# Optimization experiments

Measured on AMD Instinct MI355X. Metric: run time of the kernel, lower is better.

## Reference

```python
import jax, jax.numpy as jnp
import numpy as np

H = 8          # num_heads
EPS = 1e-5     # nn.LayerNorm default eps


def _attn(x, kv, wq, bq, wk, bk, wv, bv, wo, bo):
    # x: [B, Nq, D] queries; kv: [B, Nk, D] keys/values. softmax over keys (dim=-1).
    B, Nq, D = x.shape
    Nk = kv.shape[1]
    d = D // H
    q = (x @ wq + bq).reshape(B, Nq, H, d).transpose(0, 2, 1, 3)   # [B,h,Nq,d]
    k = (kv @ wk + bk).reshape(B, Nk, H, d).transpose(0, 2, 1, 3)  # [B,h,Nk,d]
    v = (kv @ wv + bv).reshape(B, Nk, H, d).transpose(0, 2, 1, 3)  # [B,h,Nk,d]
    scores = jnp.einsum('bhqd,bhkd->bhqk', q, k) * (d ** -0.5)
    a = jax.nn.softmax(scores, axis=-1)                            # softmax_dim='keys'
    ctx = jnp.einsum('bhqk,bhkd->bhqd', a, v)
    ctx = ctx.transpose(0, 2, 1, 3).reshape(B, Nq, D)
    return ctx @ wo + bo


def _ln(x, g, b):
    mu = jnp.mean(x, axis=-1, keepdims=True)
    var = jnp.var(x, axis=-1, keepdims=True)  # biased, matches torch LayerNorm
    return (x - mu) * jax.lax.rsqrt(var + EPS) * g + b


def setup_inputs() -> dict:
    key = jax.random.key(0)
    B, Nq, Nk, D = 2, 2048, 4096, 512
    Hid = 4 * D
    ks = jax.random.split(key, 32)
    s = 0.02
    r = lambda i, shp: jax.random.normal(ks[i], shp, dtype=jnp.float32) * s
    inp = {
        'x': jax.random.normal(ks[0], (B, Nq, D), dtype=jnp.float32),
        'cross': jax.random.normal(ks[1], (B, Nk, D), dtype=jnp.float32),
        # cross-attention projections (stored as [in, out])
        'ca_wq': r(2, (D, D)), 'ca_bq': jnp.zeros((D,), jnp.float32),
        'ca_wk': r(3, (D, D)), 'ca_bk': jnp.zeros((D,), jnp.float32),
        'ca_wv': r(4, (D, D)), 'ca_bv': jnp.zeros((D,), jnp.float32),
        'ca_wo': r(5, (D, D)), 'ca_bo': jnp.zeros((D,), jnp.float32),
        # self-attention projections
        'sa_wq': r(6, (D, D)), 'sa_bq': jnp.zeros((D,), jnp.float32),
        'sa_wk': r(7, (D, D)), 'sa_bk': jnp.zeros((D,), jnp.float32),
        'sa_wv': r(8, (D, D)), 'sa_bv': jnp.zeros((D,), jnp.float32),
        'sa_wo': r(9, (D, D)), 'sa_bo': jnp.zeros((D,), jnp.float32),
        # layer norms
        'ln1_g': jnp.ones((D,), jnp.float32), 'ln1_b': jnp.zeros((D,), jnp.float32),
        'ln2_g': jnp.ones((D,), jnp.float32), 'ln2_b': jnp.zeros((D,), jnp.float32),
        # MLP
        'mlp_w1': r(10, (D, Hid)), 'mlp_b1': jnp.zeros((Hid,), jnp.float32),
        'mlp_w2': r(11, (Hid, D)), 'mlp_b2': jnp.zeros((D,), jnp.float32),
    }
    return inp


def reference(x, cross,
              ca_wq, ca_bq, ca_wk, ca_bk, ca_wv, ca_bv, ca_wo, ca_bo,
              sa_wq, sa_bq, sa_wk, sa_bk, sa_wv, sa_bv, sa_wo, sa_bo,
              ln1_g, ln1_b, ln2_g, ln2_b,
              mlp_w1, mlp_b1, mlp_w2, mlp_b2):
    # a) cross-attention
    xc = _attn(x, cross, ca_wq, ca_bq, ca_wk, ca_bk, ca_wv, ca_bv, ca_wo, ca_bo)
    # b,c) LN then self-attention (Q=K=V=ln1(xc))
    xn = _ln(xc, ln1_g, ln1_b)
    xs = _attn(xn, xn, sa_wq, sa_bq, sa_wk, sa_bk, sa_wv, sa_bv, sa_wo, sa_bo)
    # d) residual
    y = xc + xs
    # e,f) LN + GELU MLP (torch GELU default = exact erf)
    h1 = jax.nn.gelu(_ln(y, ln2_g, ln2_b) @ mlp_w1 + mlp_b1, approximate=False)
    z = h1 @ mlp_w2 + mlp_b2
    # g) residual
    return y + z
```

## Files before the change

### kernel.cpp

```cpp
#include <hip/hip_runtime.h>
#include <math.h>

typedef _Float16 f16;
typedef __attribute__((ext_vector_type(8))) _Float16 f16x8;
typedef __attribute__((ext_vector_type(4))) _Float16 f16x4;
typedef __attribute__((ext_vector_type(4))) float f32x4;
typedef __attribute__((ext_vector_type(2))) __fp16 h16x2;

#define QSCALE 0.1803368801111204f

__device__ __forceinline__ void gl_lds16(const f16* g, f16* l) {
    __builtin_amdgcn_global_load_lds((const __attribute__((address_space(1))) void*)g,
                                     (__attribute__((address_space(3))) void*)l, 16, 0, 0);
}

__global__ __launch_bounds__(256)
void cvt_f16_kernel(const float* __restrict__ X, f16* __restrict__ Y) {
    size_t i = ((size_t)blockIdx.x * 256 + threadIdx.x) * 4;
    f32x4 v = *(const f32x4*)(X + i);
    f16x4 o;
    o[0] = (f16)v[0]; o[1] = (f16)v[1]; o[2] = (f16)v[2]; o[3] = (f16)v[3];
    *(f16x4*)(Y + i) = o;
}

__global__ __launch_bounds__(256)
void transpose_cvt(const float* __restrict__ W, f16* __restrict__ Wt, int K, int N) {
    __shared__ float t[32][33];
    int tx = threadIdx.x, ty = threadIdx.y;
    int n0 = blockIdx.x * 32, k0 = blockIdx.y * 32;
#pragma unroll
    for (int i = 0; i < 4; i++)
        t[ty + i * 8][tx] = W[(size_t)(k0 + ty + i * 8) * N + n0 + tx];
    __syncthreads();
#pragma unroll
    for (int i = 0; i < 4; i++)
        Wt[(size_t)(n0 + ty + i * 8) * K + k0 + tx] = (f16)t[tx][ty + i * 8];
}

struct P8 { const float* s[8]; f16* d[8]; };
__global__ __launch_bounds__(256)
void transpose_cvt8(P8 p) {
    __shared__ float t[32][33];
    const float* W = p.s[blockIdx.z];
    f16* Wt = p.d[blockIdx.z];
    int tx = threadIdx.x, ty = threadIdx.y;
    int n0 = blockIdx.x * 32, k0 = blockIdx.y * 32;
#pragma unroll
    for (int i = 0; i < 4; i++)
        t[ty + i * 8][tx] = W[(size_t)(k0 + ty + i * 8) * 512 + n0 + tx];
    __syncthreads();
#pragma unroll
    for (int i = 0; i < 4; i++)
        Wt[(size_t)(n0 + ty + i * 8) * 512 + k0 + tx] = (f16)t[tx][ty + i * 8];
}

__global__ __launch_bounds__(256)
void transpose_v(const f16* __restrict__ Vh, f16* __restrict__ Vt, int Nk) {
    __shared__ f16 t[64][72];
    int bh = blockIdx.y, k0 = blockIdx.x * 64;
    int tid = threadIdx.x;
    int kr = tid >> 2, dc = (tid & 3) * 16;
    const f16* src = Vh + ((size_t)bh * Nk + k0 + kr) * 64 + dc;
    f16x8 a = *(const f16x8*)src;
    f16x8 b = *(const f16x8*)(src + 8);
    *(f16x8*)&t[kr][dc] = a;
    *(f16x8*)&t[kr][dc + 8] = b;
    __syncthreads();
    int dr = tid >> 2, kc = (tid & 3) * 16;
    f16x8 o0, o1;
#pragma unroll
    for (int j = 0; j < 8; j++) { o0[j] = t[kc + j][dr]; o1[j] = t[kc + 8 + j][dr]; }
    f16* dst = Vt + ((size_t)bh * 64 + dr) * Nk + k0 + kc;
    *(f16x8*)dst = o0;
    *(f16x8*)(dst + 8) = o1;
}

__global__ __launch_bounds__(128)
void layernorm_f16(const float* __restrict__ X, const float* __restrict__ g,
                   const float* __restrict__ bta, f16* __restrict__ Y)
{
    __shared__ float red[4];
    int row = blockIdx.x;
    int tid = threadIdx.x;
    const float* x = X + (size_t)row * 512;
    f32x4 v = *(const f32x4*)(x + tid * 4);
    float s  = v[0] + v[1] + v[2] + v[3];
    float ss = v[0] * v[0] + v[1] * v[1] + v[2] * v[2] + v[3] * v[3];
#pragma unroll
    for (int m = 1; m < 64; m <<= 1) {
        s  += __shfl_xor(s, m, 64);
        ss += __shfl_xor(ss, m, 64);
    }
    int wave = tid >> 6, lane = tid & 63;
    if (lane == 0) { red[wave * 2] = s; red[wave * 2 + 1] = ss; }
    __syncthreads();
    s = red[0] + red[2]; ss = red[1] + red[3];
    float mu  = s * (1.0f / 512);
    float var = ss * (1.0f / 512) - mu * mu;
    float inv = rsqrtf(var + 1e-5f);
    f32x4 gv = *(const f32x4*)(g + tid * 4);
    f32x4 bv = *(const f32x4*)(bta + tid * 4);
    f16x4 o;
#pragma unroll
    for (int i = 0; i < 4; i++) o[i] = (f16)((v[i] - mu) * inv * gv[i] + bv[i]);
    *(f16x4*)(Y + (size_t)row * 512 + tid * 4) = o;
}

__global__ __launch_bounds__(256)
void gemm_f16(const f16* __restrict__ A, const f16* __restrict__ Wt,
              const float* __restrict__ b0, const float* __restrict__ b1,
              const float* __restrict__ b2, const float* __restrict__ res,
              float* __restrict__ Cf32, f16* __restrict__ C16,
              f16* __restrict__ hm0, f16* __restrict__ hm1, f16* __restrict__ hm2,
              int N, int K, int NBshift, int fused, int act, float s0)
{
    __shared__ __align__(16) f16 As[128 * 64];
    __shared__ __align__(16) f16 Bs[128 * 64];
    int tid = threadIdx.x, lane = tid & 63, wave = tid >> 6;
    int quad = lane >> 4, ln16 = lane & 15;
    int wm = wave >> 1, wn = wave & 1;
    int bm0 = blockIdx.y * 128, bn0 = blockIdx.x * 128;

    f32x4 acc[4][4];
#pragma unroll
    for (int i = 0; i < 4; i++)
#pragma unroll
        for (int j = 0; j < 4; j++) acc[i][j] = (f32x4){0.f, 0.f, 0.f, 0.f};

    const f16* ag[4]; const f16* bg[4]; f16* al[4]; f16* bl[4];
#pragma unroll
    for (int j = 0; j < 4; j++) {
        int L = tid + j * 256;
        int row = L >> 3, cc = (L & 7) ^ (row & 7);
        ag[j] = A  + (size_t)(bm0 + row) * K + cc * 8;
        bg[j] = Wt + (size_t)(bn0 + row) * K + cc * 8;
        al[j] = As + (size_t)L * 8;
        bl[j] = Bs + (size_t)L * 8;
    }
    int sw0 = (quad ^ (ln16 & 7)) * 8, sw1 = ((4 + quad) ^ (ln16 & 7)) * 8;

    for (int kt = 0; kt < K; kt += 64) {
        __syncthreads();
#pragma unroll
        for (int j = 0; j < 4; j++) gl_lds16(ag[j], al[j]);
#pragma unroll
        for (int j = 0; j < 4; j++) gl_lds16(bg[j], bl[j]);
        __syncthreads();
#pragma unroll
        for (int h = 0; h < 2; h++) {
            int sw = h ? sw1 : sw0;
            f16x8 af[4], bf[4];
#pragma unroll
            for (int mt = 0; mt < 4; mt++)
                af[mt] = *(const f16x8*)&As[(wm * 64 + mt * 16 + ln16) * 64 + sw];
#pragma unroll
            for (int nt = 0; nt < 4; nt++)
                bf[nt] = *(const f16x8*)&Bs[(wn * 64 + nt * 16 + ln16) * 64 + sw];
#pragma unroll
            for (int mt = 0; mt < 4; mt++)
#pragma unroll
                for (int nt = 0; nt < 4; nt++)
                    acc[mt][nt] = __builtin_amdgcn_mfma_f32_16x16x32_f16(af[mt], bf[nt], acc[mt][nt], 0, 0, 0);
        }
#pragma unroll
        for (int j = 0; j < 4; j++) { ag[j] += 64; bg[j] += 64; }
    }

    int NB = 1 << NBshift;
#pragma unroll
    for (int mt = 0; mt < 4; mt++) {
#pragma unroll
        for (int nt = 0; nt < 4; nt++) {
            int row = bm0 + wm * 64 + mt * 16 + quad * 4;
            int col = bn0 + wn * 64 + nt * 16 + ln16;
            float bv;
            if (fused) {
                int seg = col >> 9;
                const float* bp = seg == 0 ? b0 : (seg == 1 ? b1 : b2);
                bv = bp[col & 511];
            } else bv = b0[col];
#pragma unroll
            for (int i = 0; i < 4; i++) {
                int r = row + i;
                float v = acc[mt][nt][i] + bv;
                size_t idx = (size_t)r * N + col;
                if (res) v += res[idx];
                if (act) v = 0.5f * v * (1.0f + erff(v * 0.70710678118654752f));
                if (Cf32) Cf32[idx] = v;
                if (C16) C16[idx] = (f16)v;
                if (hm0) {
                    int seg = col >> 9;
                    f16* hp = seg == 0 ? hm0 : (seg == 1 ? hm1 : hm2);
                    float vv = seg == 0 ? v * s0 : v;
                    int hh = (col >> 6) & 7, d = col & 63;
                    int bt = r >> NBshift, rr = r & (NB - 1);
                    hp[(((size_t)bt * 8 + hh) * NB + rr) * 64 + d] = (f16)vv;
                }
            }
        }
    }
}

__global__ __launch_bounds__(256)
void gemm64(const f16* __restrict__ A, const f16* __restrict__ Wt,
            const float* __restrict__ bias, const float* __restrict__ res,
            float* __restrict__ Cf32, f16* __restrict__ hm0,
            int N, int K, int NBshift, float s0)
{
    __shared__ __align__(16) f16 As[64 * 64];
    __shared__ __align__(16) f16 Bs[64 * 64];
    int tid = threadIdx.x, lane = tid & 63, wave = tid >> 6;
    int quad = lane >> 4, ln16 = lane & 15;
    int wm = wave >> 1, wn = wave & 1;
    int bm0 = blockIdx.y * 64, bn0 = blockIdx.x * 64;

    f32x4 acc[2][2];
#pragma unroll
    for (int i = 0; i < 2; i++)
#pragma unroll
        for (int j = 0; j < 2; j++) acc[i][j] = (f32x4){0.f, 0.f, 0.f, 0.f};

    const f16* ag[2]; const f16* bg[2]; f16* al[2]; f16* bl[2];
#pragma unroll
    for (int j = 0; j < 2; j++) {
        int L = tid + j * 256;
        int row = L >> 3, cc = (L & 7) ^ (row & 7);
        ag[j] = A  + (size_t)(bm0 + row) * K + cc * 8;
        bg[j] = Wt + (size_t)(bn0 + row) * K + cc * 8;
        al[j] = As + (size_t)L * 8;
        bl[j] = Bs + (size_t)L * 8;
    }
    int sw0 = (quad ^ (ln16 & 7)) * 8, sw1 = ((4 + quad) ^ (ln16 & 7)) * 8;

    for (int kt = 0; kt < K; kt += 64) {
        __syncthreads();
#pragma unroll
        for (int j = 0; j < 2; j++) gl_lds16(ag[j], al[j]);
#pragma unroll
        for (int j = 0; j < 2; j++) gl_lds16(bg[j], bl[j]);
        __syncthreads();
#pragma unroll
        for (int h = 0; h < 2; h++) {
            int sw = h ? sw1 : sw0;
            f16x8 af[2], bf[2];
#pragma unroll
            for (int mt = 0; mt < 2; mt++)
                af[mt] = *(const f16x8*)&As[(wm * 32 + mt * 16 + ln16) * 64 + sw];
#pragma unroll
            for (int nt = 0; nt < 2; nt++)
                bf[nt] = *(const f16x8*)&Bs[(wn * 32 + nt * 16 + ln16) * 64 + sw];
#pragma unroll
            for (int mt = 0; mt < 2; mt++)
#pragma unroll
                for (int nt = 0; nt < 2; nt++)
                    acc[mt][nt] = __builtin_amdgcn_mfma_f32_16x16x32_f16(af[mt], bf[nt], acc[mt][nt], 0, 0, 0);
        }
#pragma unroll
        for (int j = 0; j < 2; j++) { ag[j] += 64; bg[j] += 64; }
    }

    int NB = 1 << NBshift;
#pragma unroll
    for (int mt = 0; mt < 2; mt++) {
#pragma unroll
        for (int nt = 0; nt < 2; nt++) {
            int row = bm0 + wm * 32 + mt * 16 + quad * 4;
            int col = bn0 + wn * 32 + nt * 16 + ln16;
            float bv = bias[col];
#pragma unroll
            for (int i = 0; i < 4; i++) {
                int r = row + i;
                float v = acc[mt][nt][i] + bv;
                size_t idx = (size_t)r * N + col;
                if (res) v += res[idx];
                if (Cf32) Cf32[idx] = v;
                if (hm0) {
                    int hh = (col >> 6) & 7, d = col & 63;
                    int bt = r >> NBshift, rr = r & (NB - 1);
                    hm0[(((size_t)bt * 8 + hh) * NB + rr) * 64 + d] = (f16)(v * s0);
                }
            }
        }
    }
}

__global__ __launch_bounds__(256, 4)
void attention_split(const f16* __restrict__ Qh, const f16* __restrict__ Kh,
                     const f16* __restrict__ Vt, f16* __restrict__ Op,
                     float* __restrict__ Lsum, int Nk)
{
    __shared__ __align__(16) f16 Kt[64 * 64];
    __shared__ __align__(16) f16 Vs[64 * 64];
    __shared__ __align__(16) f16 Ps[4 * 32 * 64];
    int z = blockIdx.z, b = z >> 2, sp = z & 3;
    int h = blockIdx.y, bh = b * 8 + h;
    int Nkh = Nk >> 2;
    int tid = threadIdx.x, lane = tid & 63, wave = tid >> 6;
    int quad = lane >> 4, ln16 = lane & 15, l7 = ln16 & 7;
    int qrow0 = blockIdx.x * 128 + wave * 32;

    f16x8 qf[2][2];
#pragma unroll
    for (int qh = 0; qh < 2; qh++)
#pragma unroll
        for (int dh = 0; dh < 2; dh++)
            qf[qh][dh] = *(const f16x8*)(Qh + ((size_t)bh * 2048 + qrow0 + qh * 16 + ln16) * 64
                                         + dh * 32 + quad * 8);
    f16x8 ones;
#pragma unroll
    for (int j = 0; j < 8; j++) ones[j] = (f16)1.0f;

    f32x4 oacc[2][4], aol[2];
#pragma unroll
    for (int qh = 0; qh < 2; qh++) {
        aol[qh] = (f32x4){0.f, 0.f, 0.f, 0.f};
#pragma unroll
        for (int dt = 0; dt < 4; dt++) oacc[qh][dt] = (f32x4){0.f, 0.f, 0.f, 0.f};
    }

    const f16* kb = Kh + ((size_t)bh * Nk + sp * Nkh) * 64;
    const f16* vb = Vt + (size_t)bh * 64 * Nk + sp * Nkh;

    const f16* kg[2]; const f16* vg[2]; f16* kl[2]; f16* vl[2];
#pragma unroll
    for (int j = 0; j < 2; j++) {
        int L = tid + j * 256;
        int row = L >> 3, cc = (L & 7) ^ (row & 7);
        kg[j] = kb + (size_t)row * 64 + cc * 8;
        vg[j] = vb + (size_t)row * Nk + cc * 8;
        kl[j] = Kt + (size_t)L * 8;
        vl[j] = Vs + (size_t)L * 8;
    }

    int koff[4][2], voff[4][2], poff_r[2][2];
#pragma unroll
    for (int nt = 0; nt < 4; nt++)
#pragma unroll
        for (int dh = 0; dh < 2; dh++)
            koff[nt][dh] = (nt * 16 + ln16) * 64 + ((dh * 4 + quad) ^ l7) * 8;
#pragma unroll
    for (int dt = 0; dt < 4; dt++)
#pragma unroll
        for (int c = 0; c < 2; c++)
            voff[dt][c] = (dt * 16 + ln16) * 64 + ((c * 4 + quad) ^ l7) * 8;
    int pbase = wave * 2048;
#pragma unroll
    for (int qh = 0; qh < 2; qh++)
#pragma unroll
        for (int c = 0; c < 2; c++)
            poff_r[qh][c] = pbase + (qh * 16 + ln16) * 64 + ((c * 4 + quad) ^ l7) * 8;
    int pw_half = (quad & 1) * 4;
    int pw_rowc = quad >> 1;

    for (int kt = 0; kt < Nkh; kt += 64) {
        __syncthreads();
#pragma unroll
        for (int j = 0; j < 2; j++) gl_lds16(kg[j], kl[j]);
#pragma unroll
        for (int j = 0; j < 2; j++) gl_lds16(vg[j], vl[j]);
        __syncthreads();
#pragma unroll
        for (int j = 0; j < 2; j++) { kg[j] += 64 * 64; vg[j] += 64; }

        {
            f16x8 kf[4][2];
#pragma unroll
            for (int nt = 0; nt < 4; nt++)
#pragma unroll
                for (int dh = 0; dh < 2; dh++)
                    kf[nt][dh] = *(const f16x8*)&Kt[koff[nt][dh]];
#pragma unroll
            for (int qh = 0; qh < 2; qh++) {
                int prow = pbase + (qh * 16 + ln16) * 64;
#pragma unroll
                for (int nt = 0; nt < 4; nt++) {
                    f32x4 zz = (f32x4){0.f, 0.f, 0.f, 0.f};
                    zz = __builtin_amdgcn_mfma_f32_16x16x32_f16(kf[nt][0], qf[qh][0], zz, 0, 0, 0);
                    zz = __builtin_amdgcn_mfma_f32_16x16x32_f16(kf[nt][1], qf[qh][1], zz, 0, 0, 0);
                    float e0 = exp2f(zz[0]), e1 = exp2f(zz[1]);
                    float e2 = exp2f(zz[2]), e3 = exp2f(zz[3]);
                    h16x2 pa = __builtin_amdgcn_cvt_pkrtz(e0, e1);
                    h16x2 pb = __builtin_amdgcn_cvt_pkrtz(e2, e3);
                    union { h16x2 h[2]; f16x4 v; } u;
                    u.h[0] = pa; u.h[1] = pb;
                    *(f16x4*)&Ps[prow + ((nt * 2 + pw_rowc) ^ l7) * 8 + pw_half] = u.v;
                }
            }
        }
        {
            f16x8 vf[4][2];
#pragma unroll
            for (int dt = 0; dt < 4; dt++)
#pragma unroll
                for (int c = 0; c < 2; c++)
                    vf[dt][c] = *(const f16x8*)&Vs[voff[dt][c]];
#pragma unroll
            for (int qh = 0; qh < 2; qh++) {
                f16x8 pf0 = *(const f16x8*)&Ps[poff_r[qh][0]];
                f16x8 pf1 = *(const f16x8*)&Ps[poff_r[qh][1]];
                aol[qh] = __builtin_amdgcn_mfma_f32_16x16x32_f16(ones, pf0, aol[qh], 0, 0, 0);
                aol[qh] = __builtin_amdgcn_mfma_f32_16x16x32_f16(ones, pf1, aol[qh], 0, 0, 0);
#pragma unroll
                for (int dt = 0; dt < 4; dt++) {
                    oacc[qh][dt] = __builtin_amdgcn_mfma_f32_16x16x32_f16(vf[dt][0], pf0, oacc[qh][dt], 0, 0, 0);
                    oacc[qh][dt] = __builtin_amdgcn_mfma_f32_16x16x32_f16(vf[dt][1], pf1, oacc[qh][dt], 0, 0, 0);
                }
            }
        }
    }

#pragma unroll
    for (int qh = 0; qh < 2; qh++) {
        size_t rowb = ((size_t)(sp * 16 + bh) * 2048 + qrow0 + qh * 16 + ln16) * 64;
#pragma unroll
        for (int dt = 0; dt < 4; dt++) {
            f16x4 o4;
#pragma unroll
            for (int i = 0; i < 4; i++) o4[i] = (f16)oacc[qh][dt][i];
            *(f16x4*)&Op[rowb + dt * 16 + quad * 4] = o4;
        }
        if (quad == 0)
            Lsum[(size_t)(sp * 16 + bh) * 2048 + qrow0 + qh * 16 + ln16] = aol[qh][0];
    }
}

__global__ __launch_bounds__(256)
void attn_combine(const f16* __restrict__ Op, const float* __restrict__ Lsum,
                  f16* __restrict__ O)
{
    int t = blockIdx.x * 256 + threadIdx.x;
    int d = t & 63;
    int q = (t >> 6) & 2047;
    int bh = t >> 17;
    int b = bh >> 3, h = bh & 7;
    float l = 0.f, val = 0.f;
#pragma unroll
    for (int s = 0; s < 4; s++) {
        l   += Lsum[(size_t)(s * 16 + bh) * 2048 + q];
        val += (float)Op[((size_t)(s * 16 + bh) * 2048 + q) * 64 + d];
    }
    O[((size_t)b * 2048 + q) * 512 + h * 64 + d] = (f16)(val / l);
}

extern "C" void kernel_launch(void* const* d_in, const int* in_sizes, int n_in,
                              void* d_out, int out_size, void* d_ws, size_t ws_size,
                              hipStream_t stream)
{
    (void)in_sizes; (void)n_in; (void)out_size; (void)ws_size;
    const float* x      = (const float*)d_in[0];
    const float* cross  = (const float*)d_in[1];
    const float* ca_wq  = (const float*)d_in[2];
    const float* ca_bq  = (const float*)d_in[3];
    const float* ca_wk  = (const float*)d_in[4];
    const float* ca_bk  = (const float*)d_in[5];
    const float* ca_wv  = (const float*)d_in[6];
    const float* ca_bv  = (const float*)d_in[7];
    const float* ca_wo  = (const float*)d_in[8];
    const float* ca_bo  = (const float*)d_in[9];
    const float* sa_wq  = (const float*)d_in[10];
    const float* sa_bq  = (const float*)d_in[11];
    const float* sa_wk  = (const float*)d_in[12];
    const float* sa_bk  = (const float*)d_in[13];
    const float* sa_wv  = (const float*)d_in[14];
    const float* sa_bv  = (const float*)d_in[15];
    const float* sa_wo  = (const float*)d_in[16];
    const float* sa_bo  = (const float*)d_in[17];
    const float* ln1_g  = (const float*)d_in[18];
    const float* ln1_b  = (const float*)d_in[19];
    const float* ln2_g  = (const float*)d_in[20];
    const float* ln2_b  = (const float*)d_in[21];
    const float* mlp_w1 = (const float*)d_in[22];
    const float* mlp_b1 = (const float*)d_in[23];
    const float* mlp_w2 = (const float*)d_in[24];
    const float* mlp_b2 = (const float*)d_in[25];
    float* out = (float*)d_out;

    float* XC = (float*)d_ws;
    float* Yb = XC + 2097152;
    f16* fb   = (f16*)(Yb + 2097152);
    f16* xh     = fb;
    f16* crossh = xh + 2097152;
    f16* xnh    = crossh + 4194304;
    f16* xn2h   = xnh + 2097152;
    f16* Qh     = xn2h + 2097152;
    f16* Kh     = Qh + 2097152;
    f16* Vh     = Kh + 4194304;
    f16* Vtb    = Vh + 4194304;
    f16* ctxh   = Vtb + 4194304;
    f16* h1h    = ctxh + 2097152;
    f16* t_caq  = h1h + 8388608;
    f16* t_cak  = t_caq + 262144;
    f16* t_cav  = t_cak + 262144;
    f16* t_cao  = t_cav + 262144;
    f16* t_saq  = t_cao + 262144;
    f16* t_sak  = t_saq + 262144;
    f16* t_sav  = t_sak + 262144;
    f16* t_sao  = t_sav + 262144;
    f16* t_w1   = t_sao + 262144;
    f16* t_w2   = t_w1 + 1048576;
    float* Lsum = (float*)(t_w2 + 1048576);

    dim3 tb(32, 8);
    P8 p8;
    p8.s[0] = ca_wq; p8.d[0] = t_caq;
    p8.s[1] = ca_wk; p8.d[1] = t_cak;
    p8.s[2] = ca_wv; p8.d[2] = t_cav;
    p8.s[3] = ca_wo; p8.d[3] = t_cao;
    p8.s[4] = sa_wq; p8.d[4] = t_saq;
    p8.s[5] = sa_wk; p8.d[5] = t_sak;
    p8.s[6] = sa_wv; p8.d[6] = t_sav;
    p8.s[7] = sa_wo; p8.d[7] = t_sao;
    transpose_cvt8<<<dim3(16, 16, 8), tb, 0, stream>>>(p8);
    transpose_cvt<<<dim3(64, 16), tb, 0, stream>>>(mlp_w1, t_w1, 512, 2048);
    transpose_cvt<<<dim3(16, 64), tb, 0, stream>>>(mlp_w2, t_w2, 2048, 512);
    cvt_f16_kernel<<<2048, 256, 0, stream>>>(x, xh);
    cvt_f16_kernel<<<4096, 256, 0, stream>>>(cross, crossh);

    gemm64<<<dim3(8, 64), 256, 0, stream>>>(xh, t_caq, ca_bq, nullptr, nullptr, Qh,
                                            512, 512, 11, QSCALE);
    gemm_f16<<<dim3(8, 64), 256, 0, stream>>>(crossh, t_cak, ca_bk, ca_bv, nullptr, nullptr,
        nullptr, nullptr, Kh, Vh, nullptr, 1024, 512, 12, 1, 0, 1.0f);
    transpose_v<<<dim3(64, 16), 256, 0, stream>>>(Vh, Vtb, 4096);
    attention_split<<<dim3(16, 8, 8), 256, 0, stream>>>(Qh, Kh, Vtb, h1h, Lsum, 4096);
    attn_combine<<<8192, 256, 0, stream>>>(h1h, Lsum, ctxh);
    gemm64<<<dim3(8, 64), 256, 0, stream>>>(ctxh, t_cao, ca_bo, nullptr, XC, nullptr,
                                            512, 512, 11, 1.0f);
    layernorm_f16<<<4096, 128, 0, stream>>>(XC, ln1_g, ln1_b, xnh);
    gemm_f16<<<dim3(12, 32), 256, 0, stream>>>(xnh, t_saq, sa_bq, sa_bk, sa_bv, nullptr,
        nullptr, nullptr, Qh, Kh, Vh, 1536, 512, 11, 1, 0, QSCALE);
    transpose_v<<<dim3(32, 16), 256, 0, stream>>>(Vh, Vtb, 2048);
    attention_split<<<dim3(16, 8, 8), 256, 0, stream>>>(Qh, Kh, Vtb, h1h, Lsum, 2048);
    attn_combine<<<8192, 256, 0, stream>>>(h1h, Lsum, ctxh);
    gemm64<<<dim3(8, 64), 256, 0, stream>>>(ctxh, t_sao, sa_bo, XC, Yb, nullptr,
                                            512, 512, 11, 1.0f);
    layernorm_f16<<<4096, 128, 0, stream>>>(Yb, ln2_g, ln2_b, xn2h);
    gemm_f16<<<dim3(16, 32), 256, 0, stream>>>(xn2h, t_w1, mlp_b1, nullptr, nullptr, nullptr,
        nullptr, h1h, nullptr, nullptr, nullptr, 2048, 512, 11, 0, 1, 1.0f);
    gemm64<<<dim3(8, 64), 256, 0, stream>>>(h1h, t_w2, mlp_b2, Yb, out, nullptr,
                                            512, 2048, 11, 1.0f);
}
```

Measured before the change: 388.5 us.

## Double-buffer LDS tiles in GEMM and attention; merge prep kernels into one launch

The GEMM and split attention kernels now use two LDS buffers. The next K/V or A/B tile is issued with global_load_lds while the current tile is consumed, leaving one barrier per iteration instead of two. This is meant to hide global-load latency behind MFMA work. The extra LDS lowers attention occupancy, with launch bounds cut from 4 to 3 blocks. Separately, the weight transpose/convert and input convert kernels are merged into a single prep_all launch to reduce launch overhead.

```diff
diff --git a/kernel.cpp b/kernel.cpp
--- a/kernel.cpp
+++ b/kernel.cpp
@@ -14,44 +14,46 @@
                                      (__attribute__((address_space(3))) void*)l, 16, 0, 0);
 }
 
+struct PrepArgs {
+    const float* ws[10]; f16* wd[10];
+    const float* x; f16* xh;
+    const float* cross; f16* ch;
+};
 __global__ __launch_bounds__(256)
-void cvt_f16_kernel(const float* __restrict__ X, f16* __restrict__ Y) {
-    size_t i = ((size_t)blockIdx.x * 256 + threadIdx.x) * 4;
-    f32x4 v = *(const f32x4*)(X + i);
-    f16x4 o;
-    o[0] = (f16)v[0]; o[1] = (f16)v[1]; o[2] = (f16)v[2]; o[3] = (f16)v[3];
-    *(f16x4*)(Y + i) = o;
-}
-
-__global__ __launch_bounds__(256)
-void transpose_cvt(const float* __restrict__ W, f16* __restrict__ Wt, int K, int N) {
+void prep_all(PrepArgs p) {
     __shared__ float t[32][33];
-    int tx = threadIdx.x, ty = threadIdx.y;
-    int n0 = blockIdx.x * 32, k0 = blockIdx.y * 32;
-#pragma unroll
-    for (int i = 0; i < 4; i++)
-        t[ty + i * 8][tx] = W[(size_t)(k0 + ty + i * 8) * N + n0 + tx];
-    __syncthreads();
-#pragma unroll
-    for (int i = 0; i < 4; i++)
-        Wt[(size_t)(n0 + ty + i * 8) * K + k0 + tx] = (f16)t[tx][ty + i * 8];
-}
-
-struct P8 { const float* s[8]; f16* d[8]; };
-__global__ __launch_bounds__(256)
-void transpose_cvt8(P8 p) {
-    __shared__ float t[32][33];
-    const float* W = p.s[blockIdx.z];
-    f16* Wt = p.d[blockIdx.z];
-    int tx = threadIdx.x, ty = threadIdx.y;
-    int n0 = blockIdx.x * 32, k0 = blockIdx.y * 32;
-#pragma unroll
-    for (int i = 0; i < 4; i++)
-        t[ty + i * 8][tx] = W[(size_t)(k0 + ty + i * 8) * 512 + n0 + tx];
-    __syncthreads();
-#pragma unroll
-    for (int i = 0; i < 4; i++)
-        Wt[(size_t)(n0 + ty + i * 8) * 512 + k0 + tx] = (f16)t[tx][ty + i * 8];
+    int bid = blockIdx.x, tid = threadIdx.x;
+    if (bid < 4096) {
+        const float* W; f16* Wt; int K, N, nx, ky;
+        if (bid < 2048) {
+            int wi = bid >> 8, tl = bid & 255;
+            W = p.ws[wi]; Wt = p.wd[wi]; K = 512; N = 512; nx = tl & 15; ky = tl >> 4;
+        } else if (bid < 3072) {
+            int tl = bid - 2048;
+            W = p.ws[8]; Wt = p.wd[8]; K = 512; N = 2048; nx = tl & 63; ky = tl >> 6;
+        } else {
+            int tl = bid - 3072;
+            W = p.ws[9]; Wt = p.wd[9]; K = 2048; N = 512; nx = tl & 15; ky = tl >> 4;
+        }
+        int tx = tid & 31, ty = tid >> 5;
+        int n0 = nx * 32, k0 = ky * 32;
+#pragma unroll
+        for (int i = 0; i < 4; i++)
+            t[ty + i * 8][tx] = W[(size_t)(k0 + ty + i * 8) * N + n0 + tx];
+        __syncthreads();
+#pragma unroll
+        for (int i = 0; i < 4; i++)
+            Wt[(size_t)(n0 + ty + i * 8) * K + k0 + tx] = (f16)t[tx][ty + i * 8];
+    } else {
+        const float* X; f16* Y; size_t cb;
+        if (bid < 6144) { X = p.x; Y = p.xh; cb = bid - 4096; }
+        else            { X = p.cross; Y = p.ch; cb = bid - 6144; }
+        size_t i = (cb * 256 + tid) * 4;
+        f32x4 v = *(const f32x4*)(X + i);
+        f16x4 o;
+        o[0] = (f16)v[0]; o[1] = (f16)v[1]; o[2] = (f16)v[2]; o[3] = (f16)v[3];
+        *(f16x4*)(Y + i) = o;
+    }
 }
 
 __global__ __launch_bounds__(256)
@@ -207,8 +209,8 @@
             float* __restrict__ Cf32, f16* __restrict__ hm0,
             int N, int K, int NBshift, float s0)
 {
-    __shared__ __align__(16) f16 As[64 * 64];
-    __shared__ __align__(16) f16 Bs[64 * 64];
+    __shared__ __align__(16) f16 As[2][64 * 64];
+    __shared__ __align__(16) f16 Bs[2][64 * 64];
     int tid = threadIdx.x, lane = tid & 63, wave = tid >> 6;
     int quad = lane >> 4, ln16 = lane & 15;
     int wm = wave >> 1, wn = wave & 1;
@@ -220,43 +222,50 @@
 #pragma unroll
         for (int j = 0; j < 2; j++) acc[i][j] = (f32x4){0.f, 0.f, 0.f, 0.f};
 
-    const f16* ag[2]; const f16* bg[2]; f16* al[2]; f16* bl[2];
+    const f16* ag[2]; const f16* bg[2]; int Loff[2];
 #pragma unroll
     for (int j = 0; j < 2; j++) {
         int L = tid + j * 256;
         int row = L >> 3, cc = (L & 7) ^ (row & 7);
         ag[j] = A  + (size_t)(bm0 + row) * K + cc * 8;
         bg[j] = Wt + (size_t)(bn0 + row) * K + cc * 8;
-        al[j] = As + (size_t)L * 8;
-        bl[j] = Bs + (size_t)L * 8;
+        Loff[j] = L * 8;
     }
     int sw0 = (quad ^ (ln16 & 7)) * 8, sw1 = ((4 + quad) ^ (ln16 & 7)) * 8;
 
+#pragma unroll
+    for (int j = 0; j < 2; j++) { gl_lds16(ag[j], &As[0][Loff[j]]); gl_lds16(bg[j], &Bs[0][Loff[j]]); }
+#pragma unroll
+    for (int j = 0; j < 2; j++) { ag[j] += 64; bg[j] += 64; }
+
+    int cur = 0;
     for (int kt = 0; kt < K; kt += 64) {
         __syncthreads();
-#pragma unroll
-        for (int j = 0; j < 2; j++) gl_lds16(ag[j], al[j]);
-#pragma unroll
-        for (int j = 0; j < 2; j++) gl_lds16(bg[j], bl[j]);
-        __syncthreads();
+        if (kt + 64 < K) {
+            int nxt = cur ^ 1;
+#pragma unroll
+            for (int j = 0; j < 2; j++) { gl_lds16(ag[j], &As[nxt][Loff[j]]); gl_lds16(bg[j], &Bs[nxt][Loff[j]]); }
+#pragma unroll
+            for (int j = 0; j < 2; j++) { ag[j] += 64; bg[j] += 64; }
+        }
+        const f16* Ac = As[cur]; const f16* Bc = Bs[cur];
 #pragma unroll
         for (int h = 0; h < 2; h++) {
             int sw = h ? sw1 : sw0;
             f16x8 af[2], bf[2];
 #pragma unroll
             for (int mt = 0; mt < 2; mt++)
-                af[mt] = *(const f16x8*)&As[(wm * 32 + mt * 16 + ln16) * 64 + sw];
+                af[mt] = *(const f16x8*)&Ac[(wm * 32 + mt * 16 + ln16) * 64 + sw];
 #pragma unroll
             for (int nt = 0; nt < 2; nt++)
-                bf[nt] = *(const f16x8*)&Bs[(wn * 32 + nt * 16 + ln16) * 64 + sw];
+                bf[nt] = *(const f16x8*)&Bc[(wn * 32 + nt * 16 + ln16) * 64 + sw];
 #pragma unroll
             for (int mt = 0; mt < 2; mt++)
 #pragma unroll
                 for (int nt = 0; nt < 2; nt++)
                     acc[mt][nt] = __builtin_amdgcn_mfma_f32_16x16x32_f16(af[mt], bf[nt], acc[mt][nt], 0, 0, 0);
         }
-#pragma unroll
-        for (int j = 0; j < 2; j++) { ag[j] += 64; bg[j] += 64; }
+        cur ^= 1;
     }
 
     int NB = 1 << NBshift;
@@ -284,13 +293,13 @@
     }
 }
 
-__global__ __launch_bounds__(256, 4)
+__global__ __launch_bounds__(256, 3)
 void attention_split(const f16* __restrict__ Qh, const f16* __restrict__ Kh,
                      const f16* __restrict__ Vt, f16* __restrict__ Op,
                      float* __restrict__ Lsum, int Nk)
 {
-    __shared__ __align__(16) f16 Kt[64 * 64];
-    __shared__ __align__(16) f16 Vs[64 * 64];
+    __shared__ __align__(16) f16 Kt[2][64 * 64];
+    __shared__ __align__(16) f16 Vs[2][64 * 64];
     __shared__ __align__(16) f16 Ps[4 * 32 * 64];
     int z = blockIdx.z, b = z >> 2, sp = z & 3;
     int h = blockIdx.y, bh = b * 8 + h;
@@ -321,15 +330,14 @@
     const f16* kb = Kh + ((size_t)bh * Nk + sp * Nkh) * 64;
     const f16* vb = Vt + (size_t)bh * 64 * Nk + sp * Nkh;
 
-    const f16* kg[2]; const f16* vg[2]; f16* kl[2]; f16* vl[2];
+    const f16* kg[2]; const f16* vg[2]; int Loff[2];
 #pragma unroll
     for (int j = 0; j < 2; j++) {
         int L = tid + j * 256;
         int row = L >> 3, cc = (L & 7) ^ (row & 7);
         kg[j] = kb + (size_t)row * 64 + cc * 8;
         vg[j] = vb + (size_t)row * Nk + cc * 8;
-        kl[j] = Kt + (size_t)L * 8;
-        vl[j] = Vs + (size_t)L * 8;
+        Loff[j] = L * 8;
     }
 
     int koff[4][2], voff[4][2], poff_r[2][2];
@@ -352,15 +360,22 @@
     int pw_half = (quad & 1) * 4;
     int pw_rowc = quad >> 1;
 
+#pragma unroll
+    for (int j = 0; j < 2; j++) { gl_lds16(kg[j], &Kt[0][Loff[j]]); gl_lds16(vg[j], &Vs[0][Loff[j]]); }
+#pragma unroll
+    for (int j = 0; j < 2; j++) { kg[j] += 64 * 64; vg[j] += 64; }
+
+    int cur = 0;
     for (int kt = 0; kt < Nkh; kt += 64) {
         __syncthreads();
-#pragma unroll
-        for (int j = 0; j < 2; j++) gl_lds16(kg[j], kl[j]);
-#pragma unroll
-        for (int j = 0; j < 2; j++) gl_lds16(vg[j], vl[j]);
-        __syncthreads();
-#pragma unroll
-        for (int j = 0; j < 2; j++) { kg[j] += 64 * 64; vg[j] += 64; }
+        if (kt + 64 < Nkh) {
+            int nxt = cur ^ 1;
+#pragma unroll
+            for (int j = 0; j < 2; j++) { gl_lds16(kg[j], &Kt[nxt][Loff[j]]); gl_lds16(vg[j], &Vs[nxt][Loff[j]]); }
+#pragma unroll
+            for (int j = 0; j < 2; j++) { kg[j] += 64 * 64; vg[j] += 64; }
+        }
+        const f16* Ktc = Kt[cur]; const f16* Vsc = Vs[cur];
 
         {
             f16x8 kf[4][2];
@@ -368,7 +383,7 @@
             for (int nt = 0; nt < 4; nt++)
 #pragma unroll
                 for (int dh = 0; dh < 2; dh++)
-                    kf[nt][dh] = *(const f16x8*)&Kt[koff[nt][dh]];
+                    kf[nt][dh] = *(const f16x8*)&Ktc[koff[nt][dh]];
 #pragma unroll
             for (int qh = 0; qh < 2; qh++) {
                 int prow = pbase + (qh * 16 + ln16) * 64;
@@ -393,7 +408,7 @@
             for (int dt = 0; dt < 4; dt++)
 #pragma unroll
                 for (int c = 0; c < 2; c++)
-                    vf[dt][c] = *(const f16x8*)&Vs[voff[dt][c]];
+                    vf[dt][c] = *(const f16x8*)&Vsc[voff[dt][c]];
 #pragma unroll
             for (int qh = 0; qh < 2; qh++) {
                 f16x8 pf0 = *(const f16x8*)&Ps[poff_r[qh][0]];
@@ -407,6 +422,7 @@
                 }
             }
         }
+        cur ^= 1;
     }
 
 #pragma unroll
@@ -500,21 +516,19 @@
     f16* t_w2   = t_w1 + 1048576;
     float* Lsum = (float*)(t_w2 + 1048576);
 
-    dim3 tb(32, 8);
-    P8 p8;
-    p8.s[0] = ca_wq; p8.d[0] = t_caq;
-    p8.s[1] = ca_wk; p8.d[1] = t_cak;
-    p8.s[2] = ca_wv; p8.d[2] = t_cav;
-    p8.s[3] = ca_wo; p8.d[3] = t_cao;
-    p8.s[4] = sa_wq; p8.d[4] = t_saq;
-    p8.s[5] = sa_wk; p8.d[5] = t_sak;
-    p8.s[6] = sa_wv; p8.d[6] = t_sav;
-    p8.s[7] = sa_wo; p8.d[7] = t_sao;
-    transpose_cvt8<<<dim3(16, 16, 8), tb, 0, stream>>>(p8);
-    transpose_cvt<<<dim3(64, 16), tb, 0, stream>>>(mlp_w1, t_w1, 512, 2048);
-    transpose_cvt<<<dim3(16, 64), tb, 0, stream>>>(mlp_w2, t_w2, 2048, 512);
-    cvt_f16_kernel<<<2048, 256, 0, stream>>>(x, xh);
-    cvt_f16_kernel<<<4096, 256, 0, stream>>>(cross, crossh);
+    PrepArgs pa;
+    pa.ws[0] = ca_wq; pa.wd[0] = t_caq;
+    pa.ws[1] = ca_wk; pa.wd[1] = t_cak;
+    pa.ws[2] = ca_wv; pa.wd[2] = t_cav;
+    pa.ws[3] = ca_wo; pa.wd[3] = t_cao;
+    pa.ws[4] = sa_wq; pa.wd[4] = t_saq;
+    pa.ws[5] = sa_wk; pa.wd[5] = t_sak;
+    pa.ws[6] = sa_wv; pa.wd[6] = t_sav;
+    pa.ws[7] = sa_wo; pa.wd[7] = t_sao;
+    pa.ws[8] = mlp_w1; pa.wd[8] = t_w1;
+    pa.ws[9] = mlp_w2; pa.wd[9] = t_w2;
+    pa.x = x; pa.xh = xh; pa.cross = cross; pa.ch = crossh;
+    prep_all<<<10240, 256, 0, stream>>>(pa);
 
     gemm64<<<dim3(8, 64), 256, 0, stream>>>(xh, t_caq, ca_bq, nullptr, nullptr, Qh,
                                             512, 512, 11, QSCALE);
```

Measured after the change: 373.8 us. 1.04x faster.
